# Kernel optimization log

Measured on AMD Instinct MI355X. Metric: run time of the kernel, lower is better.

## Reference

```python
import jax, jax.numpy as jnp
import numpy as np

B, L, DIM, HEADS = 2, 2048, 1536, 12
HD = DIM // HEADS  # 128
C = HD // 2        # 64 rotary pairs
EPS = 1e-6


def setup_inputs() -> dict:
    key = jax.random.key(0)
    ks = jax.random.split(key, 8)
    x = jax.random.normal(ks[0], (B, L, DIM), jnp.float32)
    # ragged grids: sample0 fills L, sample1 has 2*24*32 = 1536 valid tokens
    grid_sizes = jnp.array([[2, 32, 32], [2, 24, 32]], dtype=jnp.int32)
    seq_lens = jnp.array([2048, 1536], dtype=jnp.int32)
    # rope freqs table [1024, C] (cos/sin of pos * inv_freq)
    pos = jnp.arange(1024, dtype=jnp.float32)[:, None]
    inv = 1.0 / (10000.0 ** (jnp.arange(C, dtype=jnp.float32) / C))
    ang = pos * inv
    freqs_cos, freqs_sin = jnp.cos(ang), jnp.sin(ang)
    init = lambda k: jax.random.normal(k, (DIM, DIM), jnp.float32) / np.sqrt(DIM)
    return dict(
        x=x, seq_lens=seq_lens, grid_sizes=grid_sizes,
        freqs_cos=freqs_cos, freqs_sin=freqs_sin,
        Wq=init(ks[1]), bq=jnp.zeros((DIM,), jnp.float32),
        Wk=init(ks[2]), bk=jnp.zeros((DIM,), jnp.float32),
        Wv=init(ks[3]), bv=jnp.zeros((DIM,), jnp.float32),
        Wo=init(ks[4]), bo=jnp.zeros((DIM,), jnp.float32),
        gq=jnp.ones((DIM,), jnp.float32), gk=jnp.ones((DIM,), jnp.float32),
    )


def _rope_one(xb, grid, cos, sin):
    # xb: [L, n, d]; grid: (f, h, w); cos/sin: [1024, C]
    f, h, w = grid[0], grid[1], grid[2]
    c = cos.shape[1]
    c2 = c // 3
    c1 = c - 2 * c2  # freqs split [c1, c2, c2] over axes (f, h, w)
    p = jnp.arange(xb.shape[0])
    hw = h * w
    valid = p < f * hw
    fi = jnp.where(valid, p // hw, 0)
    hi = jnp.where(valid, (p // w) % h, 0)
    wi = jnp.where(valid, p % w, 0)
    cos_p = jnp.concatenate([cos[fi, :c1], cos[hi, c1:c1 + c2], cos[wi, c1 + c2:]], axis=-1)
    sin_p = jnp.concatenate([sin[fi, :c1], sin[hi, c1:c1 + c2], sin[wi, c1 + c2:]], axis=-1)
    # positions beyond seq_len pass through unrotated (identity rotation)
    cos_p = jnp.where(valid[:, None], cos_p, 1.0)[:, None, :]  # [L,1,C]
    sin_p = jnp.where(valid[:, None], sin_p, 0.0)[:, None, :]
    xr, xi = xb[..., 0::2], xb[..., 1::2]
    out_r = xr * cos_p - xi * sin_p
    out_i = xr * sin_p + xi * cos_p
    return jnp.stack([out_r, out_i], axis=-1).reshape(xb.shape)


_rope_apply = jax.vmap(_rope_one, in_axes=(0, 0, None, None))


def _rms(t, g):
    t32 = t.astype(jnp.float32)
    return (t32 * jax.lax.rsqrt(jnp.mean(t32 * t32, axis=-1, keepdims=True) + EPS) * g).astype(t.dtype)


def reference(x, seq_lens, grid_sizes, freqs_cos, freqs_sin,
              Wq, bq, Wk, bk, Wv, bv, Wo, bo, gq, gk):
    b, s = x.shape[:2]
    n, d = HEADS, HD
    q = _rms(x @ Wq + bq, gq).reshape(b, s, n, d)
    k = _rms(x @ Wk + bk, gk).reshape(b, s, n, d)
    v = (x @ Wv + bv).reshape(b, s, n, d)
    q = _rope_apply(q, grid_sizes, freqs_cos, freqs_sin)
    k = _rope_apply(k, grid_sizes, freqs_cos, freqs_sin)
    scale = 1.0 / np.sqrt(d).astype(np.float32)
    scores = jnp.einsum('bqnd,bknd->bnqk', q, k) * scale
    kmask = jnp.arange(s)[None, :] < seq_lens[:, None]  # [b, s] key validity
    scores = jnp.where(kmask[:, None, None, :], scores, jnp.float32(-1e9))
    attn = jax.nn.softmax(scores, axis=-1)
    out = jnp.einsum('bnqk,bknd->bqnd', attn, v).reshape(b, s, n * d)
    return out @ Wo + bo
```

## Files before the change

### kernel.cpp

```cpp
#include <hip/hip_runtime.h>
#include <hip/hip_bf16.h>

#define DIM   1536
#define HEADS 12
#define HD    128
#define LSEQ  2048
#define NB    2
#define NTOK  (NB*LSEQ)

using f32x4  = __attribute__((ext_vector_type(4))) float;
using f32x16 = __attribute__((ext_vector_type(16))) float;
using s16x8  = __attribute__((ext_vector_type(8))) short;
using u16x4  = __attribute__((ext_vector_type(4))) unsigned short;

__device__ __forceinline__ unsigned short f2bf(float f) {
  unsigned int u = __builtin_bit_cast(unsigned int, f);
  u += 0x7fffu + ((u >> 16) & 1u);
  return (unsigned short)(u >> 16);
}
__device__ __forceinline__ float bf2f(unsigned short u) {
  return __builtin_bit_cast(float, (unsigned int)u << 16);
}
__device__ __forceinline__ unsigned pk2(float a, float b) {
  unsigned r;
  asm("v_cvt_pk_bf16_f32 %0, %1, %2" : "=v"(r) : "v"(a), "v"(b));
  return r;
}
__device__ __forceinline__ unsigned long long pack4bf(float a, float b, float c, float d) {
  return (unsigned long long)f2bf(a) | ((unsigned long long)f2bf(b) << 16) |
         ((unsigned long long)f2bf(c) << 32) | ((unsigned long long)f2bf(d) << 48);
}
__device__ __forceinline__ void plswap(unsigned &x, unsigned &y) {
  asm volatile("v_permlane32_swap_b32 %0, %1" : "+v"(x), "+v"(y));
}
__device__ __forceinline__ void gload_lds16(const void* g, void* l) {
  __builtin_amdgcn_global_load_lds(
      (__attribute__((address_space(1))) void*)const_cast<void*>(g),
      (__attribute__((address_space(3))) void*)l,
      16, 0, 0);
}

__global__ __launch_bounds__(256) void cvt_x(const float* __restrict__ x,
                                             unsigned short* __restrict__ xb, int n) {
  int i = (blockIdx.x * 256 + threadIdx.x) * 4;
  int stride = gridDim.x * 256 * 4;
  for (; i < n; i += stride) {
    f32x4 v = *(const f32x4*)(x + i);
    u16x4 o;
    o[0] = f2bf(v[0]); o[1] = f2bf(v[1]); o[2] = f2bf(v[2]); o[3] = f2bf(v[3]);
    *(u16x4*)(xb + i) = o;
  }
}

__global__ __launch_bounds__(256) void wtrans(const float* W0, const float* W1,
                                              const float* W2, const float* W3,
                                              unsigned short* __restrict__ Wt) {
  const float* W = blockIdx.z == 0 ? W0 : blockIdx.z == 1 ? W1 : blockIdx.z == 2 ? W2 : W3;
  unsigned short* out = Wt + (size_t)blockIdx.z * DIM * DIM;
  const int n0 = blockIdx.x * 64, k0 = blockIdx.y * 64;
  __shared__ unsigned short t[64][68];
  const int tid = threadIdx.x;
#pragma unroll
  for (int i = 0; i < 16; i++) {
    int idx = tid + i * 256;
    int r = idx >> 6, c = idx & 63;
    t[r][c] = f2bf(W[(size_t)(k0 + r) * DIM + n0 + c]);
  }
  __syncthreads();
#pragma unroll
  for (int i = 0; i < 16; i++) {
    int idx = tid + i * 256;
    int r = idx >> 6, c = idx & 63;
    out[(size_t)(n0 + r) * DIM + k0 + c] = t[c][r];
  }
}

__global__ __launch_bounds__(256) void gemm_bt(
    const unsigned short* __restrict__ A, const unsigned short* __restrict__ Bt,
    void* __restrict__ Cv,
    const float* __restrict__ b0, const float* __restrict__ b1, const float* __restrict__ b2,
    int M, int N, int K, int biasMode, int outBf16) {
  __shared__ __align__(16) unsigned short As[128 * 64];
  __shared__ __align__(16) unsigned short Bs[128 * 64];
  const int tid = threadIdx.x;
  const int lane = tid & 63, w = tid >> 6;
  const int wr = w >> 1, wc = w & 1;
  const int l15 = lane & 15, g4 = lane >> 4;
  const int nwg = gridDim.x * gridDim.y;
  const int bidf = blockIdx.y * gridDim.x + blockIdx.x;
  const int cpx = nwg >> 3;
  const int sw = (bidf & 7) * cpx + (bidf >> 3);
  const int m0 = (sw / gridDim.x) * 128, n0 = (sw % gridDim.x) * 128;

  f32x4 acc[4][4];
#pragma unroll
  for (int i = 0; i < 4; i++)
#pragma unroll
    for (int j = 0; j < 4; j++) acc[i][j] = (f32x4){0.f, 0.f, 0.f, 0.f};

  for (int kt = 0; kt < K; kt += 64) {
    __syncthreads();
#pragma unroll
    for (int i = 0; i < 4; i++) {
      int c = tid + i * 256;
      int row = c >> 3, g = c & 7;
      int gs = g ^ (row & 7);
      gload_lds16(A + (size_t)(m0 + row) * K + kt + gs * 8, As + c * 8);
    }
#pragma unroll
    for (int i = 0; i < 4; i++) {
      int c = tid + i * 256;
      int row = c >> 3, g = c & 7;
      int gs = g ^ (row & 7);
      gload_lds16(Bt + (size_t)(n0 + row) * K + kt + gs * 8, Bs + c * 8);
    }
    __syncthreads();
#pragma unroll
    for (int kk = 0; kk < 2; kk++) {
      s16x8 af[4], bfr[4];
#pragma unroll
      for (int m = 0; m < 4; m++) {
        int row = wr * 64 + m * 16 + l15;
        int off = row * 128 + ((kk * 64 + g4 * 16) ^ ((row & 7) << 4));
        af[m] = *(const s16x8*)((const char*)As + off);
      }
#pragma unroll
      for (int n = 0; n < 4; n++) {
        int row = wc * 64 + n * 16 + l15;
        int off = row * 128 + ((kk * 64 + g4 * 16) ^ ((row & 7) << 4));
        bfr[n] = *(const s16x8*)((const char*)Bs + off);
      }
#pragma unroll
      for (int m = 0; m < 4; m++)
#pragma unroll
        for (int n = 0; n < 4; n++)
          acc[m][n] = __builtin_amdgcn_mfma_f32_16x16x32_bf16(af[m], bfr[n], acc[m][n], 0, 0, 0);
    }
  }
#pragma unroll
  for (int m = 0; m < 4; m++)
#pragma unroll
    for (int n = 0; n < 4; n++)
#pragma unroll
      for (int r = 0; r < 4; r++) {
        int grow = m0 + wr * 64 + m * 16 + g4 * 4 + r;
        int gcol = n0 + wc * 64 + n * 16 + l15;
        float bias = (biasMode == 1)
                         ? b0[gcol]
                         : (gcol < 1536 ? b0[gcol]
                                        : (gcol < 3072 ? b1[gcol - 1536] : b2[gcol - 3072]));
        float val = acc[m][n][r] + bias;
        if (outBf16) ((unsigned short*)Cv)[(size_t)grow * N + gcol] = f2bf(val);
        else         ((float*)Cv)[(size_t)grow * N + gcol] = val;
      }
}

__global__ __launch_bounds__(256) void rmsrope(
    const unsigned short* __restrict__ qkvb,
    const float* __restrict__ gq, const float* __restrict__ gk,
    const int* __restrict__ grid_sizes,
    const float* __restrict__ fcos, const float* __restrict__ fsin,
    unsigned short* __restrict__ qb, unsigned short* __restrict__ kb) {
  const int t = blockIdx.x;
  const int b = t >> 11, l = t & 2047;
  const int tid = threadIdx.x;
  __shared__ float qrow[1536], krow[1536];
  __shared__ float red[8];
  const unsigned short* rq = qkvb + (size_t)t * 4608;
  const unsigned short* rk = rq + 1536;
  float sq = 0.f, sk = 0.f;
  if (tid < 192) {
    s16x8 vq = *(const s16x8*)(rq + tid * 8);
    s16x8 vk = *(const s16x8*)(rk + tid * 8);
#pragma unroll
    for (int j = 0; j < 8; j++) {
      float a = bf2f((unsigned short)vq[j]); qrow[tid * 8 + j] = a; sq += a * a;
      float c = bf2f((unsigned short)vk[j]); krow[tid * 8 + j] = c; sk += c * c;
    }
  }
  for (int o = 32; o; o >>= 1) { sq += __shfl_down(sq, o); sk += __shfl_down(sk, o); }
  if ((tid & 63) == 0) { red[tid >> 6] = sq; red[4 + (tid >> 6)] = sk; }
  __syncthreads();
  const float rsq = rsqrtf((red[0] + red[1] + red[2] + red[3]) * (1.f / 1536.f) + 1e-6f);
  const float rsk = rsqrtf((red[4] + red[5] + red[6] + red[7]) * (1.f / 1536.f) + 1e-6f);
  const float QS = 0.08838834764831845f * 1.4426950408889634f;
  const int fg = grid_sizes[b * 3 + 0], hg = grid_sizes[b * 3 + 1], wg = grid_sizes[b * 3 + 2];
  const int hw = hg * wg;
  const bool valid = l < fg * hw;
  const int fi = valid ? l / hw : 0;
  const int hi = valid ? (l / wg) % hg : 0;
  const int wi = valid ? l % wg : 0;
  const size_t obase = (((size_t)b * HEADS) * LSEQ + l) * HD;
  for (int i = tid; i < HEADS * 64; i += 256) {
    int hd = i >> 6, j = i & 63;
    float c, s;
    if (valid) {
      int idx = j < 22 ? fi : (j < 43 ? hi : wi);
      c = fcos[idx * 64 + j]; s = fsin[idx * 64 + j];
    } else { c = 1.f; s = 0.f; }
    int col = hd * 128 + 2 * j;
    size_t o = obase + (size_t)hd * LSEQ * HD + 2 * j;
    float xr = qrow[col] * rsq * gq[col];
    float xi = qrow[col + 1] * rsq * gq[col + 1];
    float q0 = (xr * c - xi * s) * QS, q1 = (xr * s + xi * c) * QS;
    *(unsigned int*)(qb + o) = (unsigned int)f2bf(q0) | ((unsigned int)f2bf(q1) << 16);
    xr = krow[col] * rsk * gk[col];
    xi = krow[col + 1] * rsk * gk[col + 1];
    *(unsigned int*)(kb + o) =
        (unsigned int)f2bf(xr * c - xi * s) | ((unsigned int)f2bf(xr * s + xi * c) << 16);
  }
}

__global__ __launch_bounds__(256) void vtrans(const unsigned short* __restrict__ qkvb,
                                              unsigned short* __restrict__ vt) {
  const int lt = blockIdx.x, h = blockIdx.y, b = blockIdx.z;
  const int l0 = lt * 64;
  __shared__ unsigned short tile[64][130];
  const int tid = threadIdx.x;
#pragma unroll
  for (int i = 0; i < 4; i++) {
    int idx = tid + i * 256;
    int tk = idx >> 4, dc = (idx & 15) * 8;
    s16x8 v = *(const s16x8*)(qkvb + (size_t)(b * 2048 + l0 + tk) * 4608 + 3072 + h * 128 + dc);
#pragma unroll
    for (int j = 0; j < 8; j++) tile[tk][dc + j] = (unsigned short)v[j];
  }
  __syncthreads();
  const size_t ob = (((size_t)b * HEADS + h) * HD) * LSEQ + l0;
#pragma unroll
  for (int i = 0; i < 4; i++) {
    int idx = tid + i * 256;
    int d = idx >> 3, ck = (idx & 7) * 8;
    s16x8 o;
#pragma unroll
    for (int j = 0; j < 8; j++) o[j] = (short)tile[ck + j][d];
    *(s16x8*)(vt + ob + (size_t)d * LSEQ + ck) = o;
  }
}

__global__ __launch_bounds__(256) void flash(
    const unsigned short* __restrict__ qb, const unsigned short* __restrict__ kb,
    const unsigned short* __restrict__ vt, const int* __restrict__ seq_lens,
    unsigned short* __restrict__ pO, float* __restrict__ pls, float* __restrict__ pm) {
  const int orig = blockIdx.x + 16 * (blockIdx.y + 12 * blockIdx.z);
  const int wg = (orig & 7) * 96 + (orig >> 3);
  const int qt = wg & 15;
  const int r4 = wg >> 4;
  const int hh = r4 % 12;
  const int z2 = r4 / 12;
  const int b = z2 >> 1, half = z2 & 1;
  const int tid = threadIdx.x, lane = tid & 63, w = tid >> 6;
  const int l31 = lane & 31, hi = lane >> 5;
  __shared__ __align__(16) unsigned short Ks[2][32 * 128];
  __shared__ __align__(16) unsigned short Vs[2][128 * 32];
  const size_t bh = (size_t)b * HEADS + hh;
  const int q0 = qt * 128 + w * 32;

  s16x8 qf[8];
  {
    const unsigned short* qp = qb + (bh * LSEQ + q0 + l31) * HD + hi * 8;
#pragma unroll
    for (int s = 0; s < 8; s++) qf[s] = *(const s16x8*)(qp + s * 16);
  }
  const int ntile = seq_lens[b] >> 5;
  const int htiles = ntile >> 1;
  const int k0t = half * htiles;
  const int kend = k0t + htiles;
  asm volatile("s_waitcnt vmcnt(0)" ::: "memory");

  f32x16 acc[4];
#pragma unroll
  for (int d = 0; d < 4; d++)
#pragma unroll
    for (int r = 0; r < 16; r++) acc[d][r] = 0.f;
  float mrow = -1e30f, ls = 0.f;

#define STAGE_K(T, BUF)                                                                \
  _Pragma("unroll") for (int i = 0; i < 2; i++) {                                      \
    int c = tid + i * 256, row = c >> 4, seg = c & 15, ss = seg ^ (row & 15);          \
    gload_lds16(kb + (bh * LSEQ + (T) * 32 + row) * HD + ss * 8, &Ks[BUF][0] + c * 8); \
  }
#define STAGE_V(T, BUF)                                                                \
  _Pragma("unroll") for (int i = 0; i < 2; i++) {                                      \
    int c = tid + i * 256, row = c >> 2, seg = c & 3, ss = seg ^ ((row >> 1) & 3);     \
    gload_lds16(vt + (bh * HD + row) * LSEQ + (T) * 32 + ss * 8, &Vs[BUF][0] + c * 8); \
  }

  STAGE_K(k0t, 0); STAGE_V(k0t, 0);
  STAGE_K(k0t + 1, 1); STAGE_V(k0t + 1, 1);

  for (int kt = k0t; kt < kend; kt++) {
    const int cur = kt & 1;
    asm volatile("s_waitcnt vmcnt(4)" ::: "memory");
    __builtin_amdgcn_s_barrier();
    __builtin_amdgcn_sched_barrier(0);
    f32x16 st0;
#pragma unroll
    for (int r = 0; r < 16; r++) st0[r] = 0.f;
    const char* ksb = (const char*)&Ks[cur][0];
    __builtin_amdgcn_s_setprio(1);
#pragma unroll
    for (int s = 0; s < 8; s++) {
      int g = 2 * s + hi;
      s16x8 kf = *(const s16x8*)(ksb + l31 * 256 + ((g ^ (l31 & 15)) << 4));
      st0 = __builtin_amdgcn_mfma_f32_32x32x16_bf16(kf, qf[s], st0, 0, 0, 0);
    }
    __builtin_amdgcn_s_setprio(0);
    f32x16 mt;
#pragma unroll
    for (int r = 0; r < 16; r++) mt[r] = st0[r];
#pragma unroll
    for (int off = 8; off; off >>= 1)
#pragma unroll
      for (int r = 0; r < off; r++) mt[r] = fmaxf(mt[r], mt[r + off]);
    float mx = fmaxf(mt[0], __shfl_xor(mt[0], 32));
    const bool grow = mx > mrow + 8.0f;
    const float alpha = grow ? exp2f(mrow - mx) : 1.f;
    if (grow) mrow = mx;
#pragma unroll
    for (int r = 0; r < 16; r++) st0[r] = exp2f(st0[r] - mrow);
    f32x16 sm;
#pragma unroll
    for (int r = 0; r < 16; r++) sm[r] = st0[r];
#pragma unroll
    for (int off = 8; off; off >>= 1)
#pragma unroll
      for (int r = 0; r < off; r++) sm[r] += sm[r + off];
    ls = ls * alpha + (sm[0] + __shfl_xor(sm[0], 32));
    if (__any((int)grow)) {
#pragma unroll
      for (int d = 0; d < 4; d++)
#pragma unroll
        for (int r = 0; r < 16; r++) acc[d][r] *= alpha;
    }
    union U { unsigned u[4]; s16x8 v; } pa0, pa1;
    {
      unsigned c0 = pk2(st0[0], st0[1]),  c1 = pk2(st0[2], st0[3]);
      unsigned c2 = pk2(st0[4], st0[5]),  c3 = pk2(st0[6], st0[7]);
      unsigned c4 = pk2(st0[8], st0[9]),  c5 = pk2(st0[10], st0[11]);
      unsigned c6 = pk2(st0[12], st0[13]), c7 = pk2(st0[14], st0[15]);
      plswap(c0, c2); plswap(c1, c3); plswap(c4, c6); plswap(c5, c7);
      pa0.u[0] = c0; pa0.u[1] = c1; pa0.u[2] = c2; pa0.u[3] = c3;
      pa1.u[0] = c4; pa1.u[1] = c5; pa1.u[2] = c6; pa1.u[3] = c7;
    }
    const char* vsb = (const char*)&Vs[cur][0];
    __builtin_amdgcn_s_setprio(1);
#pragma unroll
    for (int slot = 0; slot < 2; slot++) {
      s16x8 pb = slot == 0 ? pa0.v : pa1.v;
      int g = 2 * slot + hi;
#pragma unroll
      for (int d = 0; d < 4; d++) {
        int row = d * 32 + l31;
        s16x8 vf = *(const s16x8*)(vsb + row * 64 + ((g ^ ((row >> 1) & 3)) << 4));
        acc[d] = __builtin_amdgcn_mfma_f32_32x32x16_bf16(vf, pb, acc[d], 0, 0, 0);
      }
    }
    __builtin_amdgcn_s_setprio(0);
    __builtin_amdgcn_s_barrier();
    __builtin_amdgcn_sched_barrier(0);
    {
      int knext = (kt + 2 < kend) ? kt + 2 : kt;
      STAGE_K(knext, cur); STAGE_V(knext, cur);
    }
  }
  asm volatile("s_waitcnt vmcnt(0)" ::: "memory");
#undef STAGE_K
#undef STAGE_V
  const int p = ((b * 12 + hh) * 16 + qt) * 2 + half;
  const int ql = w * 32 + l31;
  unsigned short* pop = pO + ((size_t)p * 128 + ql) * 128 + hi * 4;
#pragma unroll
  for (int d = 0; d < 4; d++)
#pragma unroll
    for (int j = 0; j < 4; j++) {
      unsigned long long pk = pack4bf(acc[d][4 * j], acc[d][4 * j + 1],
                                      acc[d][4 * j + 2], acc[d][4 * j + 3]);
      *(unsigned long long*)(pop + d * 32 + 8 * j) = pk;
    }
  if (hi == 0) {
    pls[(size_t)p * 128 + ql] = ls;
    pm[(size_t)p * 128 + ql] = mrow;
  }
}

__global__ __launch_bounds__(256) void merge(
    const unsigned short* __restrict__ pO, const float* __restrict__ pls,
    const float* __restrict__ pm, unsigned short* __restrict__ ob) {
  const int qt = blockIdx.x, h = blockIdx.y, b = blockIdx.z;
  const int p0 = ((b * 12 + h) * 16 + qt) * 2;
  const int tid = threadIdx.x;
#pragma unroll
  for (int i = tid; i < 2048; i += 256) {
    int q = i >> 4, c = (i & 15) * 8;
    float m0 = pm[(size_t)p0 * 128 + q],  m1 = pm[(size_t)(p0 + 1) * 128 + q];
    float l0 = pls[(size_t)p0 * 128 + q], l1 = pls[(size_t)(p0 + 1) * 128 + q];
    float m = fmaxf(m0, m1);
    float a0 = exp2f(m0 - m), a1 = exp2f(m1 - m);
    float inv = 1.f / (a0 * l0 + a1 * l1);
    a0 *= inv; a1 *= inv;
    s16x8 o0 = *(const s16x8*)(pO + ((size_t)p0 * 128 + q) * 128 + c);
    s16x8 o1 = *(const s16x8*)(pO + ((size_t)(p0 + 1) * 128 + q) * 128 + c);
    s16x8 o;
#pragma unroll
    for (int j = 0; j < 8; j++)
      o[j] = (short)f2bf(bf2f((unsigned short)o0[j]) * a0 + bf2f((unsigned short)o1[j]) * a1);
    *(s16x8*)(ob + ((size_t)(b * LSEQ) + qt * 128 + q) * DIM + h * HD + c) = o;
  }
}

extern "C" void kernel_launch(void* const* d_in, const int* in_sizes, int n_in,
                              void* d_out, int out_size, void* d_ws, size_t ws_size,
                              hipStream_t stream) {
  const float* x    = (const float*)d_in[0];
  const int*   seq  = (const int*)d_in[1];
  const int*   grids= (const int*)d_in[2];
  const float* fcos = (const float*)d_in[3];
  const float* fsin = (const float*)d_in[4];
  const float* Wq   = (const float*)d_in[5];
  const float* bq   = (const float*)d_in[6];
  const float* Wk   = (const float*)d_in[7];
  const float* bk   = (const float*)d_in[8];
  const float* Wv   = (const float*)d_in[9];
  const float* bv   = (const float*)d_in[10];
  const float* Wo   = (const float*)d_in[11];
  const float* bo   = (const float*)d_in[12];
  const float* gq   = (const float*)d_in[13];
  const float* gk   = (const float*)d_in[14];

  char* ws = (char*)d_ws;
  unsigned short* xb   = (unsigned short*)(ws);
  unsigned short* Wt   = (unsigned short*)(ws + 12582912);
  unsigned short* qkvb = (unsigned short*)(ws + 31457280);
  unsigned short* qbb  = (unsigned short*)(ws + 69206016);
  unsigned short* kbb  = (unsigned short*)(ws + 81788928);
  unsigned short* pO   = (unsigned short*)(ws + 31457280);
  float*          pls  = (float*)(ws + 31457280 + 25165824);
  float*          pm   = (float*)(ws + 31457280 + 25165824 + 393216);
  unsigned short* vt   = (unsigned short*)d_out;
  unsigned short* obb  = xb;
  float* out = (float*)d_out;

  cvt_x<<<1024, 256, 0, stream>>>(x, xb, NTOK * DIM);
  wtrans<<<dim3(24, 24, 4), 256, 0, stream>>>(Wq, Wk, Wv, Wo, Wt);
  gemm_bt<<<dim3(36, 32), 256, 0, stream>>>(xb, Wt, qkvb, bq, bk, bv, NTOK, 3 * DIM, DIM, 0, 1);
  rmsrope<<<NTOK, 256, 0, stream>>>(qkvb, gq, gk, grids, fcos, fsin, qbb, kbb);
  vtrans<<<dim3(32, 12, 2), 256, 0, stream>>>(qkvb, vt);
  flash<<<dim3(16, 12, 4), 256, 0, stream>>>(qbb, kbb, vt, seq, pO, pls, pm);
  merge<<<dim3(16, 12, 2), 256, 0, stream>>>(pO, pls, pm, obb);
  gemm_bt<<<dim3(12, 32), 256, 0, stream>>>(obb, Wt + (size_t)3 * DIM * DIM, out,
                                            bo, bo, bo, NTOK, DIM, DIM, 1, 0);
}
```

Before: 245.7 us.

## Replace 128x128 GEMM with double-buffered 256x256 tile, 512-thread pipelined kernel

Swaps the GEMM used for the QKV and output projections for a new kernel. It uses 256x256 output tiles, 8 waves per block and double-buffered LDS split into two k-halves. Global-to-LDS loads for the next k-tile are issued between MFMA groups, with partial vmcnt waits and s_setprio around the MFMA bursts, so memory traffic overlaps compute and data reuse per load improves. The larger tiles mean far fewer workgroups: 288 for QKV and only 96 for the output projection. That risks a wave-quantisation tail and idle CUs on a 256-CU part.

```diff
diff --git a/kernel.cpp b/kernel.cpp
--- a/kernel.cpp
+++ b/kernel.cpp
@@ -75,75 +75,117 @@
   }
 }
 
-__global__ __launch_bounds__(256) void gemm_bt(
+__global__ __launch_bounds__(512, 1) void gemm256(
     const unsigned short* __restrict__ A, const unsigned short* __restrict__ Bt,
     void* __restrict__ Cv,
     const float* __restrict__ b0, const float* __restrict__ b1, const float* __restrict__ b2,
     int M, int N, int K, int biasMode, int outBf16) {
-  __shared__ __align__(16) unsigned short As[128 * 64];
-  __shared__ __align__(16) unsigned short Bs[128 * 64];
+  __shared__ __align__(16) unsigned short As[2][2][256 * 32];
+  __shared__ __align__(16) unsigned short Bs[2][2][256 * 32];
   const int tid = threadIdx.x;
-  const int lane = tid & 63, w = tid >> 6;
-  const int wr = w >> 1, wc = w & 1;
+  const int lane = tid & 63;
   const int l15 = lane & 15, g4 = lane >> 4;
+  const int wid = tid >> 6, wr = wid >> 2, wc = wid & 3;
   const int nwg = gridDim.x * gridDim.y;
   const int bidf = blockIdx.y * gridDim.x + blockIdx.x;
   const int cpx = nwg >> 3;
   const int sw = (bidf & 7) * cpx + (bidf >> 3);
-  const int m0 = (sw / gridDim.x) * 128, n0 = (sw % gridDim.x) * 128;
-
-  f32x4 acc[4][4];
-#pragma unroll
-  for (int i = 0; i < 4; i++)
+  const int m0 = (sw / gridDim.x) * 256, n0 = (sw % gridDim.x) * 256;
+
+  f32x4 acc[8][4];
+#pragma unroll
+  for (int i = 0; i < 8; i++)
 #pragma unroll
     for (int j = 0; j < 4; j++) acc[i][j] = (f32x4){0.f, 0.f, 0.f, 0.f};
 
-  for (int kt = 0; kt < K; kt += 64) {
-    __syncthreads();
-#pragma unroll
-    for (int i = 0; i < 4; i++) {
-      int c = tid + i * 256;
-      int row = c >> 3, g = c & 7;
-      int gs = g ^ (row & 7);
-      gload_lds16(A + (size_t)(m0 + row) * K + kt + gs * 8, As + c * 8);
-    }
-#pragma unroll
-    for (int i = 0; i < 4; i++) {
-      int c = tid + i * 256;
-      int row = c >> 3, g = c & 7;
-      int gs = g ^ (row & 7);
-      gload_lds16(Bt + (size_t)(n0 + row) * K + kt + gs * 8, Bs + c * 8);
-    }
-    __syncthreads();
-#pragma unroll
-    for (int kk = 0; kk < 2; kk++) {
-      s16x8 af[4], bfr[4];
-#pragma unroll
-      for (int m = 0; m < 4; m++) {
-        int row = wr * 64 + m * 16 + l15;
-        int off = row * 128 + ((kk * 64 + g4 * 16) ^ ((row & 7) << 4));
-        af[m] = *(const s16x8*)((const char*)As + off);
-      }
-#pragma unroll
-      for (int n = 0; n < 4; n++) {
-        int row = wc * 64 + n * 16 + l15;
-        int off = row * 128 + ((kk * 64 + g4 * 16) ^ ((row & 7) << 4));
-        bfr[n] = *(const s16x8*)((const char*)Bs + off);
-      }
-#pragma unroll
-      for (int m = 0; m < 4; m++)
-#pragma unroll
-        for (int n = 0; n < 4; n++)
-          acc[m][n] = __builtin_amdgcn_mfma_f32_16x16x32_bf16(af[m], bfr[n], acc[m][n], 0, 0, 0);
-    }
-  }
-#pragma unroll
-  for (int m = 0; m < 4; m++)
+#define SG_A(T, BUF, KH)                                                               \
+  _Pragma("unroll") for (int i = 0; i < 2; i++) {                                      \
+    int cc = tid + i * 512, row = cc >> 2, ch = cc & 3, gs = ch ^ (row & 3);           \
+    gload_lds16(A + (size_t)(m0 + row) * K + (T) * 64 + (KH) * 32 + gs * 8,            \
+                &As[BUF][KH][0] + cc * 8);                                             \
+  }
+#define SG_B(T, BUF, KH)                                                               \
+  _Pragma("unroll") for (int i = 0; i < 2; i++) {                                      \
+    int cc = tid + i * 512, row = cc >> 2, ch = cc & 3, gs = ch ^ (row & 3);           \
+    gload_lds16(Bt + (size_t)(n0 + row) * K + (T) * 64 + (KH) * 32 + gs * 8,           \
+                &Bs[BUF][KH][0] + cc * 8);                                             \
+  }
+#define RD(BASE, R) \
+  (*(const s16x8*)((BASE) + (R) * 64 + ((g4 * 16) ^ (((R) & 3) << 4))))
+
+  const int NT = K >> 6;
+  SG_A(0, 0, 0); SG_B(0, 0, 0); SG_A(0, 0, 1); SG_B(0, 0, 1);
+
+  for (int T = 0; T < NT; T++) {
+    const int c = T & 1, nc = c ^ 1;
+    const int Tn = (T + 1 < NT) ? T + 1 : T;
+    const char* a0 = (const char*)&As[c][0][0];
+    const char* a1 = (const char*)&As[c][1][0];
+    const char* bb0 = (const char*)&Bs[c][0][0];
+    const char* bb1 = (const char*)&Bs[c][1][0];
+    s16x8 af[4], bf[4];
+    SG_A(Tn, nc, 0);
+    asm volatile("s_waitcnt vmcnt(6)" ::: "memory");
+    __builtin_amdgcn_s_barrier();
+    __builtin_amdgcn_sched_barrier(0);
+#pragma unroll
+    for (int m = 0; m < 4; m++) { int lr = wr * 128 + m * 16 + l15; af[m] = RD(a0, lr); }
+#pragma unroll
+    for (int n = 0; n < 4; n++) { int rb = wc * 64 + n * 16 + l15; bf[n] = RD(bb0, rb); }
+    __builtin_amdgcn_s_setprio(1);
+#pragma unroll
+    for (int m = 0; m < 4; m++)
+#pragma unroll
+      for (int n = 0; n < 4; n++)
+        acc[m][n] = __builtin_amdgcn_mfma_f32_16x16x32_bf16(af[m], bf[n], acc[m][n], 0, 0, 0);
+    __builtin_amdgcn_s_setprio(0);
+    SG_B(Tn, nc, 0);
+#pragma unroll
+    for (int m = 0; m < 4; m++) { int lr = wr * 128 + (m + 4) * 16 + l15; af[m] = RD(a0, lr); }
+    __builtin_amdgcn_s_setprio(1);
+#pragma unroll
+    for (int m = 0; m < 4; m++)
+#pragma unroll
+      for (int n = 0; n < 4; n++)
+        acc[m + 4][n] = __builtin_amdgcn_mfma_f32_16x16x32_bf16(af[m], bf[n], acc[m + 4][n], 0, 0, 0);
+    __builtin_amdgcn_s_setprio(0);
+    SG_A(Tn, nc, 1);
+    asm volatile("s_waitcnt vmcnt(6)" ::: "memory");
+    __builtin_amdgcn_s_barrier();
+    __builtin_amdgcn_sched_barrier(0);
+#pragma unroll
+    for (int m = 0; m < 4; m++) { int lr = wr * 128 + m * 16 + l15; af[m] = RD(a1, lr); }
+#pragma unroll
+    for (int n = 0; n < 4; n++) { int rb = wc * 64 + n * 16 + l15; bf[n] = RD(bb1, rb); }
+    __builtin_amdgcn_s_setprio(1);
+#pragma unroll
+    for (int m = 0; m < 4; m++)
+#pragma unroll
+      for (int n = 0; n < 4; n++)
+        acc[m][n] = __builtin_amdgcn_mfma_f32_16x16x32_bf16(af[m], bf[n], acc[m][n], 0, 0, 0);
+    __builtin_amdgcn_s_setprio(0);
+    SG_B(Tn, nc, 1);
+#pragma unroll
+    for (int m = 0; m < 4; m++) { int lr = wr * 128 + (m + 4) * 16 + l15; af[m] = RD(a1, lr); }
+    __builtin_amdgcn_s_setprio(1);
+#pragma unroll
+    for (int m = 0; m < 4; m++)
+#pragma unroll
+      for (int n = 0; n < 4; n++)
+        acc[m + 4][n] = __builtin_amdgcn_mfma_f32_16x16x32_bf16(af[m], bf[n], acc[m + 4][n], 0, 0, 0);
+    __builtin_amdgcn_s_setprio(0);
+  }
+  asm volatile("s_waitcnt vmcnt(0)" ::: "memory");
+#undef SG_A
+#undef SG_B
+#undef RD
+#pragma unroll
+  for (int m = 0; m < 8; m++)
 #pragma unroll
     for (int n = 0; n < 4; n++)
 #pragma unroll
       for (int r = 0; r < 4; r++) {
-        int grow = m0 + wr * 64 + m * 16 + g4 * 4 + r;
+        int grow = m0 + wr * 128 + m * 16 + g4 * 4 + r;
         int gcol = n0 + wc * 64 + n * 16 + l15;
         float bias = (biasMode == 1)
                          ? b0[gcol]
@@ -443,11 +485,11 @@
 
   cvt_x<<<1024, 256, 0, stream>>>(x, xb, NTOK * DIM);
   wtrans<<<dim3(24, 24, 4), 256, 0, stream>>>(Wq, Wk, Wv, Wo, Wt);
-  gemm_bt<<<dim3(36, 32), 256, 0, stream>>>(xb, Wt, qkvb, bq, bk, bv, NTOK, 3 * DIM, DIM, 0, 1);
+  gemm256<<<dim3(18, 16), 512, 0, stream>>>(xb, Wt, qkvb, bq, bk, bv, NTOK, 3 * DIM, DIM, 0, 1);
   rmsrope<<<NTOK, 256, 0, stream>>>(qkvb, gq, gk, grids, fcos, fsin, qbb, kbb);
   vtrans<<<dim3(32, 12, 2), 256, 0, stream>>>(qkvb, vt);
   flash<<<dim3(16, 12, 4), 256, 0, stream>>>(qbb, kbb, vt, seq, pO, pls, pm);
   merge<<<dim3(16, 12, 2), 256, 0, stream>>>(pO, pls, pm, obb);
-  gemm_bt<<<dim3(12, 32), 256, 0, stream>>>(obb, Wt + (size_t)3 * DIM * DIM, out,
-                                            bo, bo, bo, NTOK, DIM, DIM, 1, 0);
-}
+  gemm256<<<dim3(6, 16), 512, 0, stream>>>(obb, Wt + (size_t)3 * DIM * DIM, out,
+                                           bo, bo, bo, NTOK, DIM, DIM, 1, 0);
+}
```

New measurement: 286.4 us. 16.6% more time.
